# Optimization experiments

Hardware: AMD Instinct MI355X
Metric: run time of the kernel (lower is better)

The kernel has to match this reference:

```python
import jax, jax.numpy as jnp
import numpy as np

B, N, H, E, V, Q = 512, 127, 256, 300, 50000, 10
DEPTH = 7          # complete binary tree of N = 2**DEPTH - 1 nodes
NN = B * N


def _tree_structure():
    # complete binary tree per sentence: node 0 = root, parent[i] = (i-1)//2
    idx = np.arange(N)
    parent = np.maximum((idx - 1) // 2, 0)              # root self-edge, masked out
    depth = np.floor(np.log2(idx + 1)).astype(np.int32)
    level = (DEPTH - 1) - depth                          # leaves -> 0, root -> DEPTH-1
    offs = np.arange(B)[:, None] * N
    parent_flat = (parent[None, :] + offs).reshape(-1).astype(np.int32)
    level_flat = np.tile(level, B).astype(np.int32)
    mask_flat = np.tile((idx != 0).astype(np.float32), B)
    return parent_flat, level_flat, mask_flat

PARENT, LEVEL, EMASK = _tree_structure()


def setup_inputs() -> dict:
    key = jax.random.key(0)
    ks = jax.random.split(key, 8)
    return {
        "tokens": jax.random.randint(ks[0], (B, N), 0, V, dtype=jnp.int32),
        "dep": jax.random.randint(ks[1], (B, N), 0, Q - 1, dtype=jnp.int32),
        "idx2vec": jax.random.normal(ks[2], (V, E), jnp.float32) * 0.1,
        "q": jax.random.normal(ks[3], (Q, H), jnp.float32) * 0.1,
        "W": jax.random.normal(ks[4], (3 * H, E), jnp.float32) * 0.05,
        "U": jax.random.normal(ks[5], (3 * H, H), jnp.float32) * 0.05,
        "D": jax.random.normal(ks[6], (3 * H, H), jnp.float32) * 0.05,
        "b": jax.random.normal(ks[7], (3 * H,), jnp.float32) * 0.05,
    }


def _forward(tokens, dep, idx2vec, q, W, U, D, b):
    parent = jnp.asarray(PARENT)
    level = jnp.asarray(LEVEL)
    emask = jnp.asarray(EMASK)[:, None]           # masks the root self-edge

    tok = tokens.reshape(-1)                      # [NN]
    dpf = dep.reshape(-1)                         # [NN] dep-type of edge to parent
    x = idx2vec[tok]                              # [NN, E]
    qc = q[dpf]                                   # [NN, H]

    Wf, Wiu = W[:H], W[H:]
    Uf, Uiu = U[:H], U[H:]
    Df, Diu = D[:H], D[H:]
    bf, biu = b[:H], b[H:]

    # per-node precomputed projections (reused across levels)
    xWf = x @ Wf.T                                # [NN, H]
    xWiu = x @ Wiu.T                              # [NN, 2H]
    qcDf = qc @ Df.T                              # [NN, H]
    qcDiu = qc @ Diu.T                            # [NN, 2H]

    # leaves: q_sum = q[-1] (leafNotion), no children, no forget term
    iu0 = xWiu + (q[-1] @ Diu.T)[None, :] + biu
    h0 = jnp.tanh(jax.nn.sigmoid(iu0[:, :H]) * jnp.tanh(iu0[:, H:]))
    h = jnp.where((level == 0)[:, None], h0, 0.0)

    # level-synchronous sweep: children are always at strictly lower levels
    for lv in range(1, DEPTH):
        hm = h * emask
        # per-child forget gate uses the PARENT's word vector (xWf gathered at parent)
        f_e = jax.nn.sigmoid(xWf[parent] + h @ Uf.T + qcDf + bf)     # [NN, H]
        f_sum = jax.ops.segment_sum(f_e * hm, parent, num_segments=NN)
        h_sum = jax.ops.segment_sum(hm, parent, num_segments=NN)
        qd_sum = jax.ops.segment_sum(qcDiu * emask, parent, num_segments=NN)
        iu = xWiu + h_sum @ Uiu.T + qd_sum + biu                     # [NN, 2H]
        h_new = jnp.tanh(jax.nn.sigmoid(iu[:, :H]) * jnp.tanh(iu[:, H:]) + f_sum)
        h = jnp.where((level == lv)[:, None], h_new, h)

    return h.reshape(B, N, H)[:, 0, :]            # root hidden state per tree


def reference(tokens, dep, idx2vec, q, W, U, D, b):
    return _forward(tokens, dep, idx2vec, q, W, U, D, b)
```

## Files before the change

kernel.cpp:

```cpp
#include <hip/hip_runtime.h>

typedef unsigned short u16;
typedef u16 u16x4 __attribute__((ext_vector_type(4)));
typedef u16 u16x8 __attribute__((ext_vector_type(8)));
typedef __bf16 bf16x8 __attribute__((ext_vector_type(8)));
typedef float f32x4 __attribute__((ext_vector_type(4)));

#define HB   256
#define NND  127
#define BT   512
#define KE   300
#define KEP  320
#define VV   50000
#define QQ   10

#define AS1 __attribute__((address_space(1)))
#define AS3 __attribute__((address_space(3)))

__device__ __forceinline__ u16 f2bf(float f) {
    unsigned int u = __builtin_bit_cast(unsigned int, f);
    u += 0x7FFFu + ((u >> 16) & 1u);
    return (u16)(u >> 16);
}
__device__ __forceinline__ float bf2f(u16 h) {
    unsigned int u = ((unsigned int)h) << 16;
    return __builtin_bit_cast(float, u);
}
__device__ __forceinline__ float sigm(float x) { return 1.f / (1.f + __expf(-x)); }

__device__ __forceinline__ void glds16(const u16* g, u16* l) {
    __builtin_amdgcn_global_load_lds((const AS1 void*)g, (AS3 void*)l, 16, 0, 0);
}

__global__ __launch_bounds__(256) void k_conv(const float* __restrict__ src,
                                              u16* __restrict__ dst) {
    long i = (long)blockIdx.x * 256 + threadIdx.x;
    int r = (int)(i / 80);
    int c = ((int)(i - (long)r * 80)) * 4;
    u16x4 o = {0, 0, 0, 0};
    if (c < KE) {
        f32x4 x = *(const f32x4*)(src + (long)r * KE + c);
#pragma unroll
        for (int e = 0; e < 4; ++e) o[e] = f2bf(x[e]);
    }
    *(u16x4*)(dst + i * 4) = o;
}

__global__ __launch_bounds__(256) void k_prep(const float* __restrict__ W,
                                              const float* __restrict__ U,
                                              const float* __restrict__ q,
                                              const float* __restrict__ D,
                                              u16* __restrict__ Wb,
                                              u16* __restrict__ Ub,
                                              float* __restrict__ qD) {
    int blk = blockIdx.x;
    if (blk < 120) {
        int i = blk * 256 + threadIdx.x;
        if (i < 768 * 40) {
            int r = i / 40, c = (i - r * 40) * 8;
            const float* s = W + (long)r * KE + c;
            u16x8 o;
#pragma unroll
            for (int e = 0; e < 8; ++e) o[e] = (c + e < KE) ? f2bf(s[e]) : (u16)0;
            *(u16x8*)(Wb + (long)i * 8) = o;
        }
    } else if (blk < 216) {
        int i = (blk - 120) * 256 + threadIdx.x;
        if (i < 768 * 32) {
            int r = i / 32, c = (i - r * 32) * 8;
            const float* s = U + (long)r * HB + c;
            u16x8 o;
#pragma unroll
            for (int e = 0; e < 8; ++e) o[e] = f2bf(s[e]);
            *(u16x8*)(Ub + (long)i * 8) = o;
        }
    } else {
        int i = (blk - 216) * 256 + threadIdx.x;
        if (i < QQ * 768) {
            int qi = i / 768, col = i - qi * 768;
            const float* qr = q + qi * HB;
            const float* dr = D + col * HB;
            float s = 0.f;
            for (int k = 0; k < HB; ++k) s += qr[k] * dr[k];
            qD[i] = s;
        }
    }
}

template <bool STORE_BF16>
__global__ __launch_bounds__(256) void k_gemm(const u16* __restrict__ A,
                                              const u16* __restrict__ B,
                                              void* __restrict__ C,
                                              int M, int N, int K,
                                              int map_cnlog2, int map_cstart) {
    __shared__ u16 As[4][128 * 32];
    __shared__ u16 Bs[4][128 * 32];

    int nwg = gridDim.x * gridDim.y;
    int orig = blockIdx.y * gridDim.x + blockIdx.x;
    int qq = nwg >> 3, rr = nwg & 7;
    int xcd = orig & 7, cidx = orig >> 3;
    int wg = (xcd < rr ? xcd * (qq + 1) : rr * (qq + 1) + (xcd - rr) * qq) + cidx;
    int bx = wg % gridDim.x, by = wg / gridDim.x;
    int row0 = by * 128, col0 = bx * 128;

    int t = threadIdx.x, lane = t & 63, w = t >> 6;
    int wr = w >> 1, wc = w & 1;

    int cof = (lane & 3) * 8;
    int rin = lane >> 2;
    int ar0 = row0 + w * 32 + rin;
    int ar1 = ar0 + 16;
    auto mapfn = [&](int r) {
        if (r > M - 1) r = M - 1;
        if (map_cnlog2 >= 0) {
            int bt = r >> map_cnlog2;
            int of = r & ((1 << map_cnlog2) - 1);
            r = bt * NND + map_cstart + of;
        }
        return r;
    };
    const u16* aS0 = A + (long)mapfn(ar0) * K + cof;
    const u16* aS1 = A + (long)mapfn(ar1) * K + cof;
    const u16* bS0 = B + (long)(col0 + w * 32 + rin) * K + cof;
    const u16* bS1 = bS0 + 16L * K;
    int dof0 = (w * 32) * 32;
    int dof1 = (w * 32 + 16) * 32;

    f32x4 acc[4][4];
#pragma unroll
    for (int m = 0; m < 4; ++m)
#pragma unroll
        for (int n = 0; n < 4; ++n) acc[m][n] = f32x4{0.f, 0.f, 0.f, 0.f};

    int arl = wr * 64 + (lane & 15);
    int brl = wc * 64 + (lane & 15);
    int kk = (lane >> 4) * 8;

    auto stage = [&](int sel, int ko) {
        glds16(aS0 + ko, &As[sel][dof0]);
        glds16(aS1 + ko, &As[sel][dof1]);
        glds16(bS0 + ko, &Bs[sel][dof0]);
        glds16(bS1 + ko, &Bs[sel][dof1]);
    };
    auto compute = [&](int sel) {
        bf16x8 af[4], bfr[4];
#pragma unroll
        for (int m = 0; m < 4; ++m)
            af[m] = *(const bf16x8*)&As[sel][(arl + m * 16) * 32 + kk];
#pragma unroll
        for (int n = 0; n < 4; ++n)
            bfr[n] = *(const bf16x8*)&Bs[sel][(brl + n * 16) * 32 + kk];
#pragma unroll
        for (int m = 0; m < 4; ++m)
#pragma unroll
            for (int n = 0; n < 4; ++n)
                acc[m][n] = __builtin_amdgcn_mfma_f32_16x16x32_bf16(af[m], bfr[n], acc[m][n], 0, 0, 0);
    };

    int nk = K >> 5;
    stage(0, 0); stage(1, 32); stage(2, 64);
    for (int kt = 0; kt < nk - 3; ++kt) {
        asm volatile("s_waitcnt vmcnt(8)" ::: "memory");
        __builtin_amdgcn_s_barrier();
        __builtin_amdgcn_sched_barrier(0);
        compute(kt & 3);
        stage((kt + 3) & 3, (kt + 3) * 32);
    }
    asm volatile("s_waitcnt vmcnt(8)" ::: "memory");
    __builtin_amdgcn_s_barrier();
    __builtin_amdgcn_sched_barrier(0);
    compute((nk - 3) & 3);
    asm volatile("s_waitcnt vmcnt(4)" ::: "memory");
    __builtin_amdgcn_s_barrier();
    __builtin_amdgcn_sched_barrier(0);
    compute((nk - 2) & 3);
    asm volatile("s_waitcnt vmcnt(0)" ::: "memory");
    __builtin_amdgcn_s_barrier();
    __builtin_amdgcn_sched_barrier(0);
    compute((nk - 1) & 3);

    int crow = row0 + wr * 64 + (lane >> 4) * 4;
    int ccol = col0 + wc * 64 + (lane & 15);
#pragma unroll
    for (int m = 0; m < 4; ++m) {
#pragma unroll
        for (int n = 0; n < 4; ++n) {
#pragma unroll
            for (int j = 0; j < 4; ++j) {
                int r = crow + m * 16 + j;
                int c = ccol + n * 16;
                if (r < M) {
                    if (STORE_BF16) ((u16*)C)[(long)r * N + c] = f2bf(acc[m][n][j]);
                    else            ((float*)C)[(long)r * N + c] = acc[m][n][j];
                }
            }
        }
    }
}

__global__ __launch_bounds__(256) void k_leaf(const int* __restrict__ tok,
                                              const u16* __restrict__ vW,
                                              const float* __restrict__ qD,
                                              const float* __restrict__ b,
                                              u16* __restrict__ h) {
    int w = threadIdx.x >> 6, t = threadIdx.x & 63;
    int leaf = blockIdx.x * 4 + w;
    int j = t * 4;
    int bt = leaf >> 6, li = leaf & 63;
    int row = bt * NND + 63 + li;
    long vwb = (long)tok[row] * 768;
    u16x4 vi = *(const u16x4*)(vW + vwb + 256 + j);
    u16x4 vu = *(const u16x4*)(vW + vwb + 512 + j);
    f32x4 qi = *(const f32x4*)(qD + 9 * 768 + 256 + j);
    f32x4 qu = *(const f32x4*)(qD + 9 * 768 + 512 + j);
    f32x4 bi = *(const f32x4*)(b + 256 + j);
    f32x4 bu = *(const f32x4*)(b + 512 + j);
    u16x4 o;
#pragma unroll
    for (int e = 0; e < 4; ++e) {
        float ii = bf2f(vi[e]) + qi[e] + bi[e];
        float uu = bf2f(vu[e]) + qu[e] + bu[e];
        o[e] = f2bf(tanhf(sigm(ii) * tanhf(uu)));
    }
    *(u16x4*)(h + (long)row * HB + j) = o;
}

__global__ __launch_bounds__(256) void k_update(const int* __restrict__ tok,
                                                const int* __restrict__ dep,
                                                const u16* __restrict__ vW,
                                                const float* __restrict__ qD,
                                                const float* __restrict__ b,
                                                const u16* __restrict__ g,
                                                u16* __restrict__ h,
                                                float* __restrict__ out,
                                                int pstart, int pnl) {
    int w = threadIdx.x >> 6, t = threadIdx.x & 63;
    int pi = blockIdx.x * 4 + w;
    int j = t * 4;
    int bt = pi >> pnl, po = pi & ((1 << pnl) - 1);
    int pl = pstart + po;
    int gp  = bt * NND + pl;
    int gc1 = bt * NND + 2 * pl + 1, gc2 = gc1 + 1;
    long cc1 = (long)((bt << (pnl + 1)) + 2 * po) * 768;
    long cc2 = cc1 + 768;
    long vwb = (long)tok[gp] * 768;
    int d1 = dep[gc1] * 768, d2 = dep[gc2] * 768;
    u16x4 vf  = *(const u16x4*)(vW + vwb + j);
    u16x4 vi  = *(const u16x4*)(vW + vwb + 256 + j);
    u16x4 vu  = *(const u16x4*)(vW + vwb + 512 + j);
    u16x4 gf1 = *(const u16x4*)(g + cc1 + j);
    u16x4 gf2 = *(const u16x4*)(g + cc2 + j);
    u16x4 gi1 = *(const u16x4*)(g + cc1 + 256 + j);
    u16x4 gi2 = *(const u16x4*)(g + cc2 + 256 + j);
    u16x4 gu1 = *(const u16x4*)(g + cc1 + 512 + j);
    u16x4 gu2 = *(const u16x4*)(g + cc2 + 512 + j);
    f32x4 qf1 = *(const f32x4*)(qD + d1 + j);
    f32x4 qf2 = *(const f32x4*)(qD + d2 + j);
    f32x4 qi1 = *(const f32x4*)(qD + d1 + 256 + j);
    f32x4 qi2 = *(const f32x4*)(qD + d2 + 256 + j);
    f32x4 qu1 = *(const f32x4*)(qD + d1 + 512 + j);
    f32x4 qu2 = *(const f32x4*)(qD + d2 + 512 + j);
    f32x4 bf_ = *(const f32x4*)(b + j);
    f32x4 bi_ = *(const f32x4*)(b + 256 + j);
    f32x4 bu_ = *(const f32x4*)(b + 512 + j);
    u16x4 h1v = *(const u16x4*)(h + (long)gc1 * HB + j);
    u16x4 h2v = *(const u16x4*)(h + (long)gc2 * HB + j);
    f32x4 res;
    u16x4 resb;
#pragma unroll
    for (int e = 0; e < 4; ++e) {
        float xf = bf2f(vf[e]) + bf_[e];
        float f1 = sigm(xf + bf2f(gf1[e]) + qf1[e]);
        float f2 = sigm(xf + bf2f(gf2[e]) + qf2[e]);
        float ii = bf2f(vi[e]) + bf2f(gi1[e]) + bf2f(gi2[e]) + qi1[e] + qi2[e] + bi_[e];
        float uu = bf2f(vu[e]) + bf2f(gu1[e]) + bf2f(gu2[e]) + qu1[e] + qu2[e] + bu_[e];
        float hn = tanhf(sigm(ii) * tanhf(uu) + f1 * bf2f(h1v[e]) + f2 * bf2f(h2v[e]));
        res[e] = hn;
        resb[e] = f2bf(hn);
    }
    if (out) *(f32x4*)(out + (long)pi * HB + j) = res;
    else     *(u16x4*)(h + (long)gp * HB + j) = resb;
}

extern "C" void kernel_launch(void* const* d_in, const int* in_sizes, int n_in,
                              void* d_out, int out_size, void* d_ws, size_t ws_size,
                              hipStream_t stream) {
    const int*   tok = (const int*)d_in[0];
    const int*   dep = (const int*)d_in[1];
    const float* vec = (const float*)d_in[2];
    const float* q   = (const float*)d_in[3];
    const float* W   = (const float*)d_in[4];
    const float* U   = (const float*)d_in[5];
    const float* D   = (const float*)d_in[6];
    const float* b   = (const float*)d_in[7];

    char* ws = (char*)d_ws;
    size_t off = 0;
    auto alloc = [&](size_t bytes) {
        void* p = ws + off;
        off += (bytes + 255) & ~(size_t)255;
        return p;
    };
    float* qD = (float*)alloc((size_t)QQ * 768 * 4);
    u16*   vb = (u16*)alloc((size_t)VV * KEP * 2);
    u16*   Wb = (u16*)alloc((size_t)768 * KEP * 2);
    u16*   Ub = (u16*)alloc((size_t)768 * HB * 2);
    u16*   vW = (u16*)alloc((size_t)VV * 768 * 2);
    u16*   h  = (u16*)alloc((size_t)BT * NND * HB * 2);
    u16*   g  = (u16*)alloc((size_t)BT * 64 * 768 * 2);
    if (ws_size < off) return;

    k_conv<<<(VV * 80) / 256, 256, 0, stream>>>(vec, vb);
    k_prep<<<246, 256, 0, stream>>>(W, U, q, D, Wb, Ub, qD);

    k_gemm<true><<<dim3(6, (VV + 127) / 128), 256, 0, stream>>>(
        vb, Wb, vW, VV, 768, KEP, -1, 0);

    k_leaf<<<BT * 64 / 4, 256, 0, stream>>>(tok, vW, qD, b, h);

    for (int lv = 1; lv <= 6; ++lv) {
        int pnl = 6 - lv;
        int pn = 1 << pnl;
        int pstart = pn - 1;
        int cnl = pnl + 1;
        int cstart = (1 << cnl) - 1;
        int npT = BT * pn, ncT = BT * (1 << cnl);
        k_gemm<true><<<dim3(6, ncT / 128), 256, 0, stream>>>(
            h, Ub, g, ncT, 768, HB, cnl, cstart);
        k_update<<<npT / 4, 256, 0, stream>>>(tok, dep, vW, qD, b, g, h,
                                              (lv == 6) ? (float*)d_out : nullptr,
                                              pstart, pnl);
    }
}
```

Before: 208.6 us.

## Fuse upper tree levels into one per-tree kernel and merge prep launches

Measured after the change: 330.3 us. 58.3% more time.

```diff
diff --git a/kernel.cpp b/kernel.cpp
--- a/kernel.cpp
+++ b/kernel.cpp
@@ -32,21 +32,9 @@
     __builtin_amdgcn_global_load_lds((const AS1 void*)g, (AS3 void*)l, 16, 0, 0);
 }
 
-__global__ __launch_bounds__(256) void k_conv(const float* __restrict__ src,
-                                              u16* __restrict__ dst) {
-    long i = (long)blockIdx.x * 256 + threadIdx.x;
-    int r = (int)(i / 80);
-    int c = ((int)(i - (long)r * 80)) * 4;
-    u16x4 o = {0, 0, 0, 0};
-    if (c < KE) {
-        f32x4 x = *(const f32x4*)(src + (long)r * KE + c);
-#pragma unroll
-        for (int e = 0; e < 4; ++e) o[e] = f2bf(x[e]);
-    }
-    *(u16x4*)(dst + i * 4) = o;
-}
-
-__global__ __launch_bounds__(256) void k_prep(const float* __restrict__ W,
+__global__ __launch_bounds__(256) void k_prep(const float* __restrict__ vec,
+                                              u16* __restrict__ vb,
+                                              const float* __restrict__ W,
                                               const float* __restrict__ U,
                                               const float* __restrict__ q,
                                               const float* __restrict__ D,
@@ -54,36 +42,41 @@
                                               u16* __restrict__ Ub,
                                               float* __restrict__ qD) {
     int blk = blockIdx.x;
-    if (blk < 120) {
-        int i = blk * 256 + threadIdx.x;
-        if (i < 768 * 40) {
-            int r = i / 40, c = (i - r * 40) * 8;
-            const float* s = W + (long)r * KE + c;
-            u16x8 o;
-#pragma unroll
-            for (int e = 0; e < 8; ++e) o[e] = (c + e < KE) ? f2bf(s[e]) : (u16)0;
-            *(u16x8*)(Wb + (long)i * 8) = o;
+    if (blk < 15625) {
+        long i = (long)blk * 256 + threadIdx.x;
+        int r = (int)(i / 80);
+        int c = ((int)(i - (long)r * 80)) * 4;
+        u16x4 o = {0, 0, 0, 0};
+        if (c < KE) {
+            f32x4 x = *(const f32x4*)(vec + (long)r * KE + c);
+#pragma unroll
+            for (int e = 0; e < 4; ++e) o[e] = f2bf(x[e]);
         }
-    } else if (blk < 216) {
-        int i = (blk - 120) * 256 + threadIdx.x;
-        if (i < 768 * 32) {
-            int r = i / 32, c = (i - r * 32) * 8;
-            const float* s = U + (long)r * HB + c;
-            u16x8 o;
-#pragma unroll
-            for (int e = 0; e < 8; ++e) o[e] = f2bf(s[e]);
-            *(u16x8*)(Ub + (long)i * 8) = o;
-        }
+        *(u16x4*)(vb + i * 4) = o;
+    } else if (blk < 15745) {
+        int i = (blk - 15625) * 256 + threadIdx.x;
+        int r = i / 40, c = (i - r * 40) * 8;
+        const float* s = W + (long)r * KE + c;
+        u16x8 o;
+#pragma unroll
+        for (int e = 0; e < 8; ++e) o[e] = (c + e < KE) ? f2bf(s[e]) : (u16)0;
+        *(u16x8*)(Wb + (long)i * 8) = o;
+    } else if (blk < 15841) {
+        int i = (blk - 15745) * 256 + threadIdx.x;
+        int r = i / 32, c = (i - r * 32) * 8;
+        const float* s = U + (long)r * HB + c;
+        u16x8 o;
+#pragma unroll
+        for (int e = 0; e < 8; ++e) o[e] = f2bf(s[e]);
+        *(u16x8*)(Ub + (long)i * 8) = o;
     } else {
-        int i = (blk - 216) * 256 + threadIdx.x;
-        if (i < QQ * 768) {
-            int qi = i / 768, col = i - qi * 768;
-            const float* qr = q + qi * HB;
-            const float* dr = D + col * HB;
-            float s = 0.f;
-            for (int k = 0; k < HB; ++k) s += qr[k] * dr[k];
-            qD[i] = s;
-        }
+        int i = (blk - 15841) * 256 + threadIdx.x;
+        int qi = i / 768, col = i - qi * 768;
+        const float* qr = q + qi * HB;
+        const float* dr = D + col * HB;
+        float s = 0.f;
+        for (int k = 0; k < HB; ++k) s += qr[k] * dr[k];
+        qD[i] = s;
     }
 }
 
@@ -233,7 +226,6 @@
                                                 const float* __restrict__ b,
                                                 const u16* __restrict__ g,
                                                 u16* __restrict__ h,
-                                                float* __restrict__ out,
                                                 int pstart, int pnl) {
     int w = threadIdx.x >> 6, t = threadIdx.x & 63;
     int pi = blockIdx.x * 4 + w;
@@ -266,7 +258,6 @@
     f32x4 bu_ = *(const f32x4*)(b + 512 + j);
     u16x4 h1v = *(const u16x4*)(h + (long)gc1 * HB + j);
     u16x4 h2v = *(const u16x4*)(h + (long)gc2 * HB + j);
-    f32x4 res;
     u16x4 resb;
 #pragma unroll
     for (int e = 0; e < 4; ++e) {
@@ -276,11 +267,111 @@
         float ii = bf2f(vi[e]) + bf2f(gi1[e]) + bf2f(gi2[e]) + qi1[e] + qi2[e] + bi_[e];
         float uu = bf2f(vu[e]) + bf2f(gu1[e]) + bf2f(gu2[e]) + qu1[e] + qu2[e] + bu_[e];
         float hn = tanhf(sigm(ii) * tanhf(uu) + f1 * bf2f(h1v[e]) + f2 * bf2f(h2v[e]));
-        res[e] = hn;
         resb[e] = f2bf(hn);
     }
-    if (out) *(f32x4*)(out + (long)pi * HB + j) = res;
-    else     *(u16x4*)(h + (long)gp * HB + j) = resb;
+    *(u16x4*)(h + (long)gp * HB + j) = resb;
+}
+
+__global__ __launch_bounds__(256) void k_tail(const int* __restrict__ tok,
+                                              const int* __restrict__ dep,
+                                              const u16* __restrict__ vW,
+                                              const float* __restrict__ qD,
+                                              const float* __restrict__ b,
+                                              const u16* __restrict__ Ub,
+                                              u16* __restrict__ h,
+                                              float* __restrict__ out) {
+    __shared__ u16 Us[384 * 32];
+    __shared__ u16 Ast[32 * 32];
+    __shared__ u16 gf[32 * 256];
+    __shared__ u16 giu[16 * 512];
+
+    int bt = blockIdx.x;
+    int t = threadIdx.x, lane = t & 63, w = t >> 6;
+    int rin = lane >> 2, cof = (lane & 3) * 8;
+    int kk = (lane >> 4) * 8;
+
+    for (int lv = 2; lv <= 6; ++lv) {
+        int pnl = 6 - lv;
+        int pn = 1 << pnl;
+        int cn = pn << 1;
+        int pstart = pn - 1, cstart = cn - 1;
+        int mt_w, ncb, nf_cnt;
+        if (cn == 32) { mt_w = w & 1; ncb = (w >> 1) * 192; nf_cnt = 12; }
+        else          { mt_w = 0;     ncb = w * 96;         nf_cnt = 6;  }
+
+        for (int pass = 0; pass < 2; ++pass) {
+            f32x4 acc[12];
+#pragma unroll
+            for (int n = 0; n < 12; ++n) acc[n] = f32x4{0.f, 0.f, 0.f, 0.f};
+
+            for (int ks = 0; ks < 8; ++ks) {
+                __syncthreads();
+#pragma unroll
+                for (int is = 0; is < 6; ++is) {
+                    int nrow = is * 64 + w * 16 + rin;
+                    glds16(Ub + (long)(pass * 384 + nrow) * HB + ks * 32 + cof,
+                           &Us[(is * 64 + w * 16) * 32]);
+                }
+                if (w < 2) {
+                    int r = w * 16 + rin;
+                    int rc = r < cn ? r : cn - 1;
+                    glds16(h + (long)(bt * NND + cstart + rc) * HB + ks * 32 + cof,
+                           &Ast[(w * 16) * 32]);
+                }
+                __syncthreads();
+                bf16x8 af = *(const bf16x8*)&Ast[(mt_w * 16 + (lane & 15)) * 32 + kk];
+#pragma unroll
+                for (int nf = 0; nf < 12; ++nf) {
+                    if (nf < nf_cnt) {
+                        bf16x8 bfr = *(const bf16x8*)&Us[(ncb + nf * 16 + (lane & 15)) * 32 + kk];
+                        acc[nf] = __builtin_amdgcn_mfma_f32_16x16x32_bf16(af, bfr, acc[nf], 0, 0, 0);
+                    }
+                }
+            }
+            int crow = mt_w * 16 + (lane >> 4) * 4;
+#pragma unroll
+            for (int nf = 0; nf < 12; ++nf) {
+                if (nf < nf_cnt && crow < cn) {
+                    int gcol = pass * 384 + ncb + nf * 16 + (lane & 15);
+                    if (gcol < 256) {
+#pragma unroll
+                        for (int j = 0; j < 4; ++j)
+                            gf[(crow + j) * 256 + gcol] = f2bf(acc[nf][j]);
+                    } else {
+                        int ci = gcol - 256;
+                        giu[(crow >> 1) * 512 + ci]       = f2bf(acc[nf][0] + acc[nf][1]);
+                        giu[((crow >> 1) + 1) * 512 + ci] = f2bf(acc[nf][2] + acc[nf][3]);
+                    }
+                }
+            }
+        }
+        __syncthreads();
+
+        int tpc = 256 / pn;
+        int p = t / tpc;
+        int c0 = (t % tpc) * pn;
+        int gp  = bt * NND + pstart + p;
+        int gc1 = bt * NND + cstart + 2 * p, gc2 = gc1 + 1;
+        long vwb = (long)tok[gp] * 768;
+        int d1 = dep[gc1] * 768, d2 = dep[gc2] * 768;
+        int c1l = 2 * p, c2l = 2 * p + 1;
+        for (int cc = 0; cc < pn; ++cc) {
+            int col = c0 + cc;
+            float xf = bf2f(vW[vwb + col]) + b[col];
+            float f1 = sigm(xf + bf2f(gf[c1l * 256 + col]) + qD[d1 + col]);
+            float f2 = sigm(xf + bf2f(gf[c2l * 256 + col]) + qD[d2 + col]);
+            float ii = bf2f(vW[vwb + 256 + col]) + bf2f(giu[p * 512 + col])
+                     + qD[d1 + 256 + col] + qD[d2 + 256 + col] + b[256 + col];
+            float uu = bf2f(vW[vwb + 512 + col]) + bf2f(giu[p * 512 + 256 + col])
+                     + qD[d1 + 512 + col] + qD[d2 + 512 + col] + b[512 + col];
+            float h1 = bf2f(h[(long)gc1 * HB + col]);
+            float h2 = bf2f(h[(long)gc2 * HB + col]);
+            float hn = tanhf(sigm(ii) * tanhf(uu) + f1 * h1 + f2 * h2);
+            if (lv == 6) out[(long)bt * HB + col] = hn;
+            else         h[(long)gp * HB + col] = f2bf(hn);
+        }
+        __syncthreads();
+    }
 }
 
 extern "C" void kernel_launch(void* const* d_in, const int* in_sizes, int n_in,
@@ -311,25 +402,17 @@
     u16*   g  = (u16*)alloc((size_t)BT * 64 * 768 * 2);
     if (ws_size < off) return;
 
-    k_conv<<<(VV * 80) / 256, 256, 0, stream>>>(vec, vb);
-    k_prep<<<246, 256, 0, stream>>>(W, U, q, D, Wb, Ub, qD);
+    k_prep<<<15871, 256, 0, stream>>>(vec, vb, W, U, q, D, Wb, Ub, qD);
 
     k_gemm<true><<<dim3(6, (VV + 127) / 128), 256, 0, stream>>>(
         vb, Wb, vW, VV, 768, KEP, -1, 0);
 
     k_leaf<<<BT * 64 / 4, 256, 0, stream>>>(tok, vW, qD, b, h);
 
-    for (int lv = 1; lv <= 6; ++lv) {
-        int pnl = 6 - lv;
-        int pn = 1 << pnl;
-        int pstart = pn - 1;
-        int cnl = pnl + 1;
-        int cstart = (1 << cnl) - 1;
-        int npT = BT * pn, ncT = BT * (1 << cnl);
-        k_gemm<true><<<dim3(6, ncT / 128), 256, 0, stream>>>(
-            h, Ub, g, ncT, 768, HB, cnl, cstart);
-        k_update<<<npT / 4, 256, 0, stream>>>(tok, dep, vW, qD, b, g, h,
-                                              (lv == 6) ? (float*)d_out : nullptr,
-                                              pstart, pnl);
-    }
-}
+    k_gemm<true><<<dim3(6, 256), 256, 0, stream>>>(
+        h, Ub, g, BT * 64, 768, HB, 6, 63);
+
+    k_update<<<BT * 32 / 4, 256, 0, stream>>>(tok, dep, vW, qD, b, g, h, 31, 5);
+
+    k_tail<<<BT, 256, 0, stream>>>(tok, dep, vW, qD, b, Ub, h, (float*)d_out);
+}
```

## Fuse per-level child GEMM with gate update and merge prep kernels

Applied to the files above, without the earlier changes.

Measured after the change: 250.0 us. 19.8% more time.

```diff
diff --git a/kernel.cpp b/kernel.cpp
--- a/kernel.cpp
+++ b/kernel.cpp
@@ -32,21 +32,9 @@
     __builtin_amdgcn_global_load_lds((const AS1 void*)g, (AS3 void*)l, 16, 0, 0);
 }
 
-__global__ __launch_bounds__(256) void k_conv(const float* __restrict__ src,
-                                              u16* __restrict__ dst) {
-    long i = (long)blockIdx.x * 256 + threadIdx.x;
-    int r = (int)(i / 80);
-    int c = ((int)(i - (long)r * 80)) * 4;
-    u16x4 o = {0, 0, 0, 0};
-    if (c < KE) {
-        f32x4 x = *(const f32x4*)(src + (long)r * KE + c);
-#pragma unroll
-        for (int e = 0; e < 4; ++e) o[e] = f2bf(x[e]);
-    }
-    *(u16x4*)(dst + i * 4) = o;
-}
-
-__global__ __launch_bounds__(256) void k_prep(const float* __restrict__ W,
+__global__ __launch_bounds__(256) void k_prep(const float* __restrict__ vec,
+                                              u16* __restrict__ vb,
+                                              const float* __restrict__ W,
                                               const float* __restrict__ U,
                                               const float* __restrict__ q,
                                               const float* __restrict__ D,
@@ -54,45 +42,48 @@
                                               u16* __restrict__ Ub,
                                               float* __restrict__ qD) {
     int blk = blockIdx.x;
-    if (blk < 120) {
-        int i = blk * 256 + threadIdx.x;
-        if (i < 768 * 40) {
-            int r = i / 40, c = (i - r * 40) * 8;
-            const float* s = W + (long)r * KE + c;
-            u16x8 o;
-#pragma unroll
-            for (int e = 0; e < 8; ++e) o[e] = (c + e < KE) ? f2bf(s[e]) : (u16)0;
-            *(u16x8*)(Wb + (long)i * 8) = o;
+    if (blk < 15625) {
+        long i = (long)blk * 256 + threadIdx.x;
+        int r = (int)(i / 80);
+        int c = ((int)(i - (long)r * 80)) * 4;
+        u16x4 o = {0, 0, 0, 0};
+        if (c < KE) {
+            f32x4 x = *(const f32x4*)(vec + (long)r * KE + c);
+#pragma unroll
+            for (int e = 0; e < 4; ++e) o[e] = f2bf(x[e]);
         }
-    } else if (blk < 216) {
-        int i = (blk - 120) * 256 + threadIdx.x;
-        if (i < 768 * 32) {
-            int r = i / 32, c = (i - r * 32) * 8;
-            const float* s = U + (long)r * HB + c;
-            u16x8 o;
-#pragma unroll
-            for (int e = 0; e < 8; ++e) o[e] = f2bf(s[e]);
-            *(u16x8*)(Ub + (long)i * 8) = o;
-        }
+        *(u16x4*)(vb + i * 4) = o;
+    } else if (blk < 15745) {
+        int i = (blk - 15625) * 256 + threadIdx.x;
+        int r = i / 40, c = (i - r * 40) * 8;
+        const float* s = W + (long)r * KE + c;
+        u16x8 o;
+#pragma unroll
+        for (int e = 0; e < 8; ++e) o[e] = (c + e < KE) ? f2bf(s[e]) : (u16)0;
+        *(u16x8*)(Wb + (long)i * 8) = o;
+    } else if (blk < 15841) {
+        int i = (blk - 15745) * 256 + threadIdx.x;
+        int r = i / 32, c = (i - r * 32) * 8;
+        const float* s = U + (long)r * HB + c;
+        u16x8 o;
+#pragma unroll
+        for (int e = 0; e < 8; ++e) o[e] = f2bf(s[e]);
+        *(u16x8*)(Ub + (long)i * 8) = o;
     } else {
-        int i = (blk - 216) * 256 + threadIdx.x;
-        if (i < QQ * 768) {
-            int qi = i / 768, col = i - qi * 768;
-            const float* qr = q + qi * HB;
-            const float* dr = D + col * HB;
-            float s = 0.f;
-            for (int k = 0; k < HB; ++k) s += qr[k] * dr[k];
-            qD[i] = s;
-        }
-    }
-}
-
-template <bool STORE_BF16>
+        int i = (blk - 15841) * 256 + threadIdx.x;
+        int qi = i / 768, col = i - qi * 768;
+        const float* qr = q + qi * HB;
+        const float* dr = D + col * HB;
+        float s = 0.f;
+        for (int k = 0; k < HB; ++k) s += qr[k] * dr[k];
+        qD[i] = s;
+    }
+}
+
 __global__ __launch_bounds__(256) void k_gemm(const u16* __restrict__ A,
                                               const u16* __restrict__ B,
-                                              void* __restrict__ C,
-                                              int M, int N, int K,
-                                              int map_cnlog2, int map_cstart) {
+                                              u16* __restrict__ C,
+                                              int M, int N, int K) {
     __shared__ u16 As[4][128 * 32];
     __shared__ u16 Bs[4][128 * 32];
 
@@ -109,19 +100,10 @@
 
     int cof = (lane & 3) * 8;
     int rin = lane >> 2;
-    int ar0 = row0 + w * 32 + rin;
-    int ar1 = ar0 + 16;
-    auto mapfn = [&](int r) {
-        if (r > M - 1) r = M - 1;
-        if (map_cnlog2 >= 0) {
-            int bt = r >> map_cnlog2;
-            int of = r & ((1 << map_cnlog2) - 1);
-            r = bt * NND + map_cstart + of;
-        }
-        return r;
-    };
-    const u16* aS0 = A + (long)mapfn(ar0) * K + cof;
-    const u16* aS1 = A + (long)mapfn(ar1) * K + cof;
+    int ar0 = row0 + w * 32 + rin; if (ar0 > M - 1) ar0 = M - 1;
+    int ar1 = row0 + w * 32 + 16 + rin; if (ar1 > M - 1) ar1 = M - 1;
+    const u16* aS0 = A + (long)ar0 * K + cof;
+    const u16* aS1 = A + (long)ar1 * K + cof;
     const u16* bS0 = B + (long)(col0 + w * 32 + rin) * K + cof;
     const u16* bS1 = bS0 + 16L * K;
     int dof0 = (w * 32) * 32;
@@ -189,11 +171,7 @@
 #pragma unroll
             for (int j = 0; j < 4; ++j) {
                 int r = crow + m * 16 + j;
-                int c = ccol + n * 16;
-                if (r < M) {
-                    if (STORE_BF16) ((u16*)C)[(long)r * N + c] = f2bf(acc[m][n][j]);
-                    else            ((float*)C)[(long)r * N + c] = acc[m][n][j];
-                }
+                if (r < M) C[(long)r * N + ccol + n * 16] = f2bf(acc[m][n][j]);
             }
         }
     }
@@ -226,61 +204,98 @@
     *(u16x4*)(h + (long)row * HB + j) = o;
 }
 
-__global__ __launch_bounds__(256) void k_update(const int* __restrict__ tok,
-                                                const int* __restrict__ dep,
-                                                const u16* __restrict__ vW,
-                                                const float* __restrict__ qD,
-                                                const float* __restrict__ b,
-                                                const u16* __restrict__ g,
-                                                u16* __restrict__ h,
-                                                float* __restrict__ out,
-                                                int pstart, int pnl) {
-    int w = threadIdx.x >> 6, t = threadIdx.x & 63;
-    int pi = blockIdx.x * 4 + w;
-    int j = t * 4;
-    int bt = pi >> pnl, po = pi & ((1 << pnl) - 1);
-    int pl = pstart + po;
-    int gp  = bt * NND + pl;
-    int gc1 = bt * NND + 2 * pl + 1, gc2 = gc1 + 1;
-    long cc1 = (long)((bt << (pnl + 1)) + 2 * po) * 768;
-    long cc2 = cc1 + 768;
-    long vwb = (long)tok[gp] * 768;
-    int d1 = dep[gc1] * 768, d2 = dep[gc2] * 768;
-    u16x4 vf  = *(const u16x4*)(vW + vwb + j);
-    u16x4 vi  = *(const u16x4*)(vW + vwb + 256 + j);
-    u16x4 vu  = *(const u16x4*)(vW + vwb + 512 + j);
-    u16x4 gf1 = *(const u16x4*)(g + cc1 + j);
-    u16x4 gf2 = *(const u16x4*)(g + cc2 + j);
-    u16x4 gi1 = *(const u16x4*)(g + cc1 + 256 + j);
-    u16x4 gi2 = *(const u16x4*)(g + cc2 + 256 + j);
-    u16x4 gu1 = *(const u16x4*)(g + cc1 + 512 + j);
-    u16x4 gu2 = *(const u16x4*)(g + cc2 + 512 + j);
-    f32x4 qf1 = *(const f32x4*)(qD + d1 + j);
-    f32x4 qf2 = *(const f32x4*)(qD + d2 + j);
-    f32x4 qi1 = *(const f32x4*)(qD + d1 + 256 + j);
-    f32x4 qi2 = *(const f32x4*)(qD + d2 + 256 + j);
-    f32x4 qu1 = *(const f32x4*)(qD + d1 + 512 + j);
-    f32x4 qu2 = *(const f32x4*)(qD + d2 + 512 + j);
-    f32x4 bf_ = *(const f32x4*)(b + j);
-    f32x4 bi_ = *(const f32x4*)(b + 256 + j);
-    f32x4 bu_ = *(const f32x4*)(b + 512 + j);
-    u16x4 h1v = *(const u16x4*)(h + (long)gc1 * HB + j);
-    u16x4 h2v = *(const u16x4*)(h + (long)gc2 * HB + j);
-    f32x4 res;
-    u16x4 resb;
-#pragma unroll
-    for (int e = 0; e < 4; ++e) {
-        float xf = bf2f(vf[e]) + bf_[e];
-        float f1 = sigm(xf + bf2f(gf1[e]) + qf1[e]);
-        float f2 = sigm(xf + bf2f(gf2[e]) + qf2[e]);
-        float ii = bf2f(vi[e]) + bf2f(gi1[e]) + bf2f(gi2[e]) + qi1[e] + qi2[e] + bi_[e];
-        float uu = bf2f(vu[e]) + bf2f(gu1[e]) + bf2f(gu2[e]) + qu1[e] + qu2[e] + bu_[e];
-        float hn = tanhf(sigm(ii) * tanhf(uu) + f1 * bf2f(h1v[e]) + f2 * bf2f(h2v[e]));
-        res[e] = hn;
-        resb[e] = f2bf(hn);
-    }
-    if (out) *(f32x4*)(out + (long)pi * HB + j) = res;
-    else     *(u16x4*)(h + (long)gp * HB + j) = resb;
+__global__ __launch_bounds__(512) void k_lvl(const int* __restrict__ tok,
+                                             const int* __restrict__ dep,
+                                             const u16* __restrict__ vW,
+                                             const float* __restrict__ qD,
+                                             const float* __restrict__ b,
+                                             const u16* __restrict__ Ub,
+                                             u16* __restrict__ h,
+                                             float* __restrict__ out,
+                                             int cnl) {
+    __shared__ u16 Bs[768 * 32];
+    __shared__ u16 As[64 * 32];
+
+    int cn = 1 << cnl, cstart = cn - 1;
+    int pnl = cnl - 1, pn = 1 << pnl, pstart = pn - 1;
+    int blk = blockIdx.x;
+    int t = threadIdx.x, lane = t & 63, w = t >> 6;
+    int rin = lane >> 2, cof = (lane & 3) * 8;
+    int kk = (lane >> 4) * 8;
+    int l15 = lane & 15;
+
+    int rhA = blk * 64 + w * 16 + rin;
+    int btA = rhA >> cnl;
+    const u16* aSrc = h + (long)(btA * NND + cstart + (rhA & (cn - 1))) * HB + cof;
+    const u16* bSrc = Ub + (long)(w * 16 + rin) * HB + cof;
+
+    f32x4 acc[4][6];
+#pragma unroll
+    for (int m = 0; m < 4; ++m)
+#pragma unroll
+        for (int f = 0; f < 6; ++f) acc[m][f] = f32x4{0.f, 0.f, 0.f, 0.f};
+
+    for (int ks = 0; ks < 8; ++ks) {
+        __syncthreads();
+        if (w < 4) glds16(aSrc + ks * 32, &As[(w * 16) * 32]);
+#pragma unroll
+        for (int is = 0; is < 6; ++is)
+            glds16(bSrc + (long)is * 128 * HB + ks * 32, &Bs[(is * 128 + w * 16) * 32]);
+        __syncthreads();
+        bf16x8 af[4], bf[6];
+#pragma unroll
+        for (int m = 0; m < 4; ++m)
+            af[m] = *(const bf16x8*)&As[(m * 16 + l15) * 32 + kk];
+#pragma unroll
+        for (int f = 0; f < 6; ++f) {
+            int part = f >> 1, within = f & 1;
+            int brow = part * 256 + w * 32 + within * 16 + l15;
+            bf[f] = *(const bf16x8*)&Bs[brow * 32 + kk];
+        }
+#pragma unroll
+        for (int m = 0; m < 4; ++m)
+#pragma unroll
+            for (int f = 0; f < 6; ++f)
+                acc[m][f] = __builtin_amdgcn_mfma_f32_16x16x32_bf16(af[m], bf[f], acc[m][f], 0, 0, 0);
+    }
+
+#pragma unroll
+    for (int m = 0; m < 4; ++m) {
+        int r0 = m * 16 + (lane >> 4) * 4;
+#pragma unroll
+        for (int qp = 0; qp < 2; ++qp) {
+            int ca = r0 + 2 * qp;
+            int rh = blk * 64 + ca;
+            int pi = rh >> 1;
+            int bt = pi >> pnl;
+            int po = pi & (pn - 1);
+            int gp  = bt * NND + pstart + po;
+            int gc1 = bt * NND + cstart + (rh & (cn - 1));
+            int gc2 = gc1 + 1;
+            long vwb = (long)tok[gp] * 768;
+            int d1 = dep[gc1] * 768, d2 = dep[gc2] * 768;
+#pragma unroll
+            for (int within = 0; within < 2; ++within) {
+                int c = w * 32 + within * 16 + l15;
+                float fe1 = acc[m][within][2 * qp];
+                float fe2 = acc[m][within][2 * qp + 1];
+                float gis = acc[m][2 + within][2 * qp] + acc[m][2 + within][2 * qp + 1];
+                float gus = acc[m][4 + within][2 * qp] + acc[m][4 + within][2 * qp + 1];
+                float xf = bf2f(vW[vwb + c]) + b[c];
+                float f1 = sigm(xf + fe1 + qD[d1 + c]);
+                float f2 = sigm(xf + fe2 + qD[d2 + c]);
+                float ii = bf2f(vW[vwb + 256 + c]) + gis
+                         + qD[d1 + 256 + c] + qD[d2 + 256 + c] + b[256 + c];
+                float uu = bf2f(vW[vwb + 512 + c]) + gus
+                         + qD[d1 + 512 + c] + qD[d2 + 512 + c] + b[512 + c];
+                float h1 = bf2f(h[(long)gc1 * HB + c]);
+                float h2 = bf2f(h[(long)gc2 * HB + c]);
+                float hn = tanhf(sigm(ii) * tanhf(uu) + f1 * h1 + f2 * h2);
+                if (out) out[(long)bt * HB + c] = hn;
+                else     h[(long)gp * HB + c] = f2bf(hn);
+            }
+        }
+    }
 }
 
 extern "C" void kernel_launch(void* const* d_in, const int* in_sizes, int n_in,
@@ -308,28 +323,18 @@
     u16*   Ub = (u16*)alloc((size_t)768 * HB * 2);
     u16*   vW = (u16*)alloc((size_t)VV * 768 * 2);
     u16*   h  = (u16*)alloc((size_t)BT * NND * HB * 2);
-    u16*   g  = (u16*)alloc((size_t)BT * 64 * 768 * 2);
     if (ws_size < off) return;
 
-    k_conv<<<(VV * 80) / 256, 256, 0, stream>>>(vec, vb);
-    k_prep<<<246, 256, 0, stream>>>(W, U, q, D, Wb, Ub, qD);
-
-    k_gemm<true><<<dim3(6, (VV + 127) / 128), 256, 0, stream>>>(
-        vb, Wb, vW, VV, 768, KEP, -1, 0);
+    k_prep<<<15871, 256, 0, stream>>>(vec, vb, W, U, q, D, Wb, Ub, qD);
+
+    k_gemm<<<dim3(6, (VV + 127) / 128), 256, 0, stream>>>(vb, Wb, vW, VV, 768, KEP);
 
     k_leaf<<<BT * 64 / 4, 256, 0, stream>>>(tok, vW, qD, b, h);
 
     for (int lv = 1; lv <= 6; ++lv) {
-        int pnl = 6 - lv;
-        int pn = 1 << pnl;
-        int pstart = pn - 1;
-        int cnl = pnl + 1;
-        int cstart = (1 << cnl) - 1;
-        int npT = BT * pn, ncT = BT * (1 << cnl);
-        k_gemm<true><<<dim3(6, ncT / 128), 256, 0, stream>>>(
-            h, Ub, g, ncT, 768, HB, cnl, cstart);
-        k_update<<<npT / 4, 256, 0, stream>>>(tok, dep, vW, qD, b, g, h,
-                                              (lv == 6) ? (float*)d_out : nullptr,
-                                              pstart, pnl);
-    }
-}
+        int cnl = 7 - lv;
+        int ncT = BT << cnl;
+        k_lvl<<<ncT / 64, 512, 0, stream>>>(tok, dep, vW, qD, b, Ub, h,
+                                            (lv == 6) ? (float*)d_out : nullptr, cnl);
+    }
+}
```
